# Performance work log

Measured on AMD Instinct MI355X. Metric: run time of the kernel, lower is better.

## Reference

```python
import jax, jax.numpy as jnp
import numpy as np

N_NODES = 40000
N_EDGES = 640000
D = 128


def setup_inputs() -> dict:
    key = jax.random.key(0)
    k1, k2, k3, k4, k5 = jax.random.split(key, 5)
    x = jax.random.normal(k1, (N_NODES, D), dtype=jnp.float32)
    edge_index = jax.random.randint(k2, (2, N_EDGES), 0, N_NODES, dtype=jnp.int64)
    # torch Linear stores weight as [out, in]; xavier ~ scaled normal
    scale = (2.0 / (D + D)) ** 0.5
    W_self = jax.random.normal(k3, (D, D), dtype=jnp.float32) * scale
    W_neigh = jax.random.normal(k4, (D, D), dtype=jnp.float32) * scale
    bias = jax.random.normal(k5, (D,), dtype=jnp.float32) * 0.01
    return {"x": x, "edge_index": edge_index, "W_self": W_self,
            "W_neigh": W_neigh, "bias": bias}


def reference(x, edge_index, W_self, W_neigh, bias):
    num_nodes = x.shape[0]
    row, col = edge_index[0], edge_index[1]
    # gather source features and scatter-add into destination nodes
    agg = jax.ops.segment_sum(x[row], col, num_segments=num_nodes)  # [N, D]
    deg = jax.ops.segment_sum(jnp.ones_like(col, dtype=x.dtype), col,
                              num_segments=num_nodes)
    agg = agg / jnp.clip(deg, 1.0)[:, None]
    # h_v = lin_self(x_v) + lin_neigh(mean_u x_u) + bias  (no activation in source)
    out = x @ W_self.T + agg @ W_neigh.T + bias
    return out
```

## Files before the change

kernel.cpp:

```cpp
#include <hip/hip_runtime.h>

#define N_NODES 40000
#define N_EDGES 640000
#define D 128
#define KCAT 256
#define CAP 64
#define NXCD 8
#define PART 5000
#define BUCKET_BLOCKS 1000
#define CHUNK_I4 1280

typedef __attribute__((ext_vector_type(8))) short short8v;
typedef __attribute__((ext_vector_type(4))) float f32x4;
typedef __attribute__((ext_vector_type(2))) float f32x2;


__device__ inline unsigned short f2bf(float f) {
  union { float f; unsigned int u; } v{f};
  unsigned int r = (v.u + 0x7FFFu + ((v.u >> 16) & 1u)) >> 16;
  return (unsigned short)r;
}

__global__ __launch_bounds__(256) void prep_count_kernel(
    const float* __restrict__ x, const float* __restrict__ Ws,
    const float* __restrict__ Wn, const int* __restrict__ ei, char* outb,
    unsigned short* __restrict__ Wcat, unsigned int* __restrict__ x8,
    int* __restrict__ deg, unsigned short* __restrict__ slot) {
  int b = blockIdx.x;
  int t = threadIdx.x;
  int tid = b * 256 + t;
  {
    int node = tid >> 5;
    int l = tid & 31;
    float4 v = *reinterpret_cast<const float4*>(x + (size_t)node * D + l * 4);
    ushort4 h;
    h.x = f2bf(v.x); h.y = f2bf(v.y); h.z = f2bf(v.z); h.w = f2bf(v.w);
    *reinterpret_cast<ushort4*>(outb + (size_t)node * 512 + l * 8) = h;
    unsigned int u = __builtin_amdgcn_cvt_pk_fp8_f32(v.x, v.y, 0, false);
    u = __builtin_amdgcn_cvt_pk_fp8_f32(v.z, v.w, u, true);
    x8[tid] = u;
  }
  if (tid < 8192) {
    int j = tid >> 6;
    int kq = tid & 63;
    int k0 = kq * 4;
    float4 v = (kq < 32)
        ? *reinterpret_cast<const float4*>(Ws + j * D + k0)
        : *reinterpret_cast<const float4*>(Wn + j * D + (k0 - D));
    ushort4 h;
    h.x = f2bf(v.x); h.y = f2bf(v.y); h.z = f2bf(v.z); h.w = f2bf(v.w);
    *reinterpret_cast<ushort4*>(Wcat + j * KCAT + k0) = h;
  }
  if (b < BUCKET_BLOCKS) {
    int p = b & (NXCD - 1);
    int chunk = b >> 3;
    int lo = p * PART;
    const int4* rq = reinterpret_cast<const int4*>(ei) + chunk * CHUNK_I4;
    const int4* cq =
        reinterpret_cast<const int4*>(ei + N_EDGES) + chunk * CHUNK_I4;
#pragma unroll
    for (int j = 0; j < 5; ++j) {
      int q = j * 256 + t;
      int4 r = rq[q];
      int4 c = cq[q];
      if ((unsigned)(c.x - lo) < PART)
        slot[(size_t)c.x * CAP + atomicAdd(&deg[c.x], 1)] = (unsigned short)r.x;
      if ((unsigned)(c.y - lo) < PART)
        slot[(size_t)c.y * CAP + atomicAdd(&deg[c.y], 1)] = (unsigned short)r.y;
      if ((unsigned)(c.z - lo) < PART)
        slot[(size_t)c.z * CAP + atomicAdd(&deg[c.z], 1)] = (unsigned short)r.z;
      if ((unsigned)(c.w - lo) < PART)
        slot[(size_t)c.w * CAP + atomicAdd(&deg[c.w], 1)] = (unsigned short)r.w;
    }
  }
}

__global__ __launch_bounds__(256) void gather_kernel(
    const unsigned int* __restrict__ x8, char* outb,
    const int* __restrict__ deg, const unsigned short* __restrict__ slot) {
  int node = blockIdx.x * 8 + (threadIdx.x >> 5);
  int l = threadIdx.x & 31;
  int nd = deg[node];
  const unsigned short* sp = slot + (size_t)node * CAP;
  float a0 = 0.f, a1 = 0.f, a2 = 0.f, a3 = 0.f;
  int e = 0;
  for (; e + 8 <= nd; e += 8) {
    unsigned int v[8];
#pragma unroll
    for (int j = 0; j < 8; ++j) v[j] = x8[(size_t)sp[e + j] * 32 + l];
#pragma unroll
    for (int j = 0; j < 8; ++j) {
      f32x2 lo = __builtin_amdgcn_cvt_pk_f32_fp8(v[j], false);
      f32x2 hi = __builtin_amdgcn_cvt_pk_f32_fp8(v[j], true);
      a0 += lo.x; a1 += lo.y; a2 += hi.x; a3 += hi.y;
    }
  }
  for (; e + 4 <= nd; e += 4) {
    unsigned int v[4];
#pragma unroll
    for (int j = 0; j < 4; ++j) v[j] = x8[(size_t)sp[e + j] * 32 + l];
#pragma unroll
    for (int j = 0; j < 4; ++j) {
      f32x2 lo = __builtin_amdgcn_cvt_pk_f32_fp8(v[j], false);
      f32x2 hi = __builtin_amdgcn_cvt_pk_f32_fp8(v[j], true);
      a0 += lo.x; a1 += lo.y; a2 += hi.x; a3 += hi.y;
    }
  }
  for (; e < nd; ++e) {
    unsigned int v = x8[(size_t)sp[e] * 32 + l];
    f32x2 lo = __builtin_amdgcn_cvt_pk_f32_fp8(v, false);
    f32x2 hi = __builtin_amdgcn_cvt_pk_f32_fp8(v, true);
    a0 += lo.x; a1 += lo.y; a2 += hi.x; a3 += hi.y;
  }
  float inv = 1.0f / fmaxf((float)nd, 1.0f);
  ushort4 h;
  h.x = f2bf(a0 * inv); h.y = f2bf(a1 * inv);
  h.z = f2bf(a2 * inv); h.w = f2bf(a3 * inv);
  *reinterpret_cast<ushort4*>(outb + (size_t)node * 512 + 256 + l * 8) = h;
}

__global__ __launch_bounds__(256) void sage_gemm_kernel(
    const char* ab, const unsigned short* __restrict__ Wcat,
    const float* __restrict__ bias, float* out) {
  __shared__ __align__(16) char Abuf[64 * 512];
  const int t = threadIdx.x;
  const int wave = t >> 6;
  const int lane = t & 63;
  const int node0 = blockIdx.x * 64;

  short8v breg[2][8];
#pragma unroll
  for (int jg = 0; jg < 2; ++jg) {
    int col = wave * 32 + jg * 16 + (lane & 15);
#pragma unroll
    for (int ks = 0; ks < 8; ++ks) {
      int k0 = ks * 32 + (lane >> 4) * 8;
      breg[jg][ks] =
          *reinterpret_cast<const short8v*>(Wcat + (size_t)col * KCAT + k0);
    }
  }

#pragma unroll
  for (int i = 0; i < 8; ++i) {
    int sl = i * 256 + t;
    int row = sl >> 5;
    int s = sl & 31;
    int4 v = *reinterpret_cast<const int4*>(
        ab + (size_t)(node0 + row) * 512 + s * 16);
    *reinterpret_cast<int4*>(Abuf + row * 512 + ((s ^ (row & 7)) << 4)) = v;
  }
  __syncthreads();

  const int srow = lane & 15;
  const int c7 = lane & 7;
  const int sb = lane >> 4;

  f32x4 acc[4][2] = {};
#pragma unroll
  for (int ks = 0; ks < 8; ++ks) {
    short8v af[4];
#pragma unroll
    for (int mf = 0; mf < 4; ++mf) {
      int row = mf * 16 + srow;
      int sl = (ks * 4 + sb) ^ c7;
      af[mf] = *reinterpret_cast<const short8v*>(Abuf + row * 512 + (sl << 4));
    }
#pragma unroll
    for (int mf = 0; mf < 4; ++mf)
#pragma unroll
      for (int jg = 0; jg < 2; ++jg)
        acc[mf][jg] = __builtin_amdgcn_mfma_f32_16x16x32_bf16(
            af[mf], breg[jg][ks], acc[mf][jg], 0, 0, 0);
  }
  __syncthreads();

#pragma unroll
  for (int jg = 0; jg < 2; ++jg) {
    int col = wave * 32 + jg * 16 + (lane & 15);
    float bv = bias[col];
#pragma unroll
    for (int mf = 0; mf < 4; ++mf) {
      int rbase = node0 + mf * 16 + (lane >> 4) * 4;
#pragma unroll
      for (int r = 0; r < 4; ++r) {
        out[(size_t)(rbase + r) * D + col] = acc[mf][jg][r] + bv;
      }
    }
  }
}

extern "C" void kernel_launch(void* const* d_in, const int* in_sizes, int n_in,
                              void* d_out, int out_size, void* d_ws, size_t ws_size,
                              hipStream_t stream) {
  const float* x    = (const float*)d_in[0];
  const int*   ei   = (const int*)d_in[1];
  const float* Ws   = (const float*)d_in[2];
  const float* Wn   = (const float*)d_in[3];
  const float* bias = (const float*)d_in[4];
  float* out = (float*)d_out;
  char* outb = (char*)d_out;

  unsigned short* Wcat = (unsigned short*)d_ws;
  int* deg = (int*)(Wcat + 128 * KCAT);
  unsigned short* slot = (unsigned short*)(deg + N_NODES);
  unsigned int* x8 =
      (unsigned int*)(slot + (size_t)N_NODES * CAP);

  hipMemsetAsync(deg, 0, N_NODES * sizeof(int), stream);
  prep_count_kernel<<<5000, 256, 0, stream>>>(x, Ws, Wn, ei, outb, Wcat, x8,
                                              deg, slot);
  gather_kernel<<<5000, 256, 0, stream>>>(x8, outb, deg, slot);
  sage_gemm_kernel<<<625, 256, 0, stream>>>(outb, Wcat, bias, out);
}
```

Baseline: 70.24 us.

## Convert x to bf16 inside the GEMM and spread edge bucketing across all blocks

```diff
diff --git a/kernel.cpp b/kernel.cpp
--- a/kernel.cpp
+++ b/kernel.cpp
@@ -7,8 +7,6 @@
 #define CAP 64
 #define NXCD 8
 #define PART 5000
-#define BUCKET_BLOCKS 1000
-#define CHUNK_I4 1280
 
 typedef __attribute__((ext_vector_type(8))) short short8v;
 typedef __attribute__((ext_vector_type(4))) float f32x4;
@@ -23,19 +21,14 @@
 
 __global__ __launch_bounds__(256) void prep_count_kernel(
     const float* __restrict__ x, const float* __restrict__ Ws,
-    const float* __restrict__ Wn, const int* __restrict__ ei, char* outb,
+    const float* __restrict__ Wn, const int* __restrict__ ei,
     unsigned short* __restrict__ Wcat, unsigned int* __restrict__ x8,
     int* __restrict__ deg, unsigned short* __restrict__ slot) {
   int b = blockIdx.x;
   int t = threadIdx.x;
   int tid = b * 256 + t;
   {
-    int node = tid >> 5;
-    int l = tid & 31;
-    float4 v = *reinterpret_cast<const float4*>(x + (size_t)node * D + l * 4);
-    ushort4 h;
-    h.x = f2bf(v.x); h.y = f2bf(v.y); h.z = f2bf(v.z); h.w = f2bf(v.w);
-    *reinterpret_cast<ushort4*>(outb + (size_t)node * 512 + l * 8) = h;
+    float4 v = *reinterpret_cast<const float4*>(x + (size_t)tid * 4);
     unsigned int u = __builtin_amdgcn_cvt_pk_fp8_f32(v.x, v.y, 0, false);
     u = __builtin_amdgcn_cvt_pk_fp8_f32(v.z, v.w, u, true);
     x8[tid] = u;
@@ -51,32 +44,26 @@
     h.x = f2bf(v.x); h.y = f2bf(v.y); h.z = f2bf(v.z); h.w = f2bf(v.w);
     *reinterpret_cast<ushort4*>(Wcat + j * KCAT + k0) = h;
   }
-  if (b < BUCKET_BLOCKS) {
+  {
     int p = b & (NXCD - 1);
     int chunk = b >> 3;
     int lo = p * PART;
-    const int4* rq = reinterpret_cast<const int4*>(ei) + chunk * CHUNK_I4;
-    const int4* cq =
-        reinterpret_cast<const int4*>(ei + N_EDGES) + chunk * CHUNK_I4;
-#pragma unroll
-    for (int j = 0; j < 5; ++j) {
-      int q = j * 256 + t;
-      int4 r = rq[q];
-      int4 c = cq[q];
-      if ((unsigned)(c.x - lo) < PART)
-        slot[(size_t)c.x * CAP + atomicAdd(&deg[c.x], 1)] = (unsigned short)r.x;
-      if ((unsigned)(c.y - lo) < PART)
-        slot[(size_t)c.y * CAP + atomicAdd(&deg[c.y], 1)] = (unsigned short)r.y;
-      if ((unsigned)(c.z - lo) < PART)
-        slot[(size_t)c.z * CAP + atomicAdd(&deg[c.z], 1)] = (unsigned short)r.z;
-      if ((unsigned)(c.w - lo) < PART)
-        slot[(size_t)c.w * CAP + atomicAdd(&deg[c.w], 1)] = (unsigned short)r.w;
-    }
+    int q = chunk * 256 + t;
+    int4 r = reinterpret_cast<const int4*>(ei)[q];
+    int4 c = reinterpret_cast<const int4*>(ei + N_EDGES)[q];
+    if ((unsigned)(c.x - lo) < PART)
+      slot[(size_t)c.x * CAP + atomicAdd(&deg[c.x], 1)] = (unsigned short)r.x;
+    if ((unsigned)(c.y - lo) < PART)
+      slot[(size_t)c.y * CAP + atomicAdd(&deg[c.y], 1)] = (unsigned short)r.y;
+    if ((unsigned)(c.z - lo) < PART)
+      slot[(size_t)c.z * CAP + atomicAdd(&deg[c.z], 1)] = (unsigned short)r.z;
+    if ((unsigned)(c.w - lo) < PART)
+      slot[(size_t)c.w * CAP + atomicAdd(&deg[c.w], 1)] = (unsigned short)r.w;
   }
 }
 
 __global__ __launch_bounds__(256) void gather_kernel(
-    const unsigned int* __restrict__ x8, char* outb,
+    const unsigned int* __restrict__ x8, unsigned short* __restrict__ aggb,
     const int* __restrict__ deg, const unsigned short* __restrict__ slot) {
   int node = blockIdx.x * 8 + (threadIdx.x >> 5);
   int l = threadIdx.x & 31;
@@ -116,12 +103,13 @@
   ushort4 h;
   h.x = f2bf(a0 * inv); h.y = f2bf(a1 * inv);
   h.z = f2bf(a2 * inv); h.w = f2bf(a3 * inv);
-  *reinterpret_cast<ushort4*>(outb + (size_t)node * 512 + 256 + l * 8) = h;
+  *reinterpret_cast<ushort4*>(aggb + (size_t)node * D + l * 4) = h;
 }
 
 __global__ __launch_bounds__(256) void sage_gemm_kernel(
-    const char* ab, const unsigned short* __restrict__ Wcat,
-    const float* __restrict__ bias, float* out) {
+    const float* __restrict__ x, const unsigned short* __restrict__ aggb,
+    const unsigned short* __restrict__ Wcat, const float* __restrict__ bias,
+    float* __restrict__ out) {
   __shared__ __align__(16) char Abuf[64 * 512];
   const int t = threadIdx.x;
   const int wave = t >> 6;
@@ -141,12 +129,27 @@
   }
 
 #pragma unroll
-  for (int i = 0; i < 8; ++i) {
-    int sl = i * 256 + t;
-    int row = sl >> 5;
-    int s = sl & 31;
-    int4 v = *reinterpret_cast<const int4*>(
-        ab + (size_t)(node0 + row) * 512 + s * 16);
+  for (int i = 0; i < 4; ++i) {
+    int q = i * 256 + t;
+    int row = q >> 4;
+    int s = q & 15;
+    const float* xp = x + (size_t)(node0 + row) * D + s * 8;
+    float4 v0 = *reinterpret_cast<const float4*>(xp);
+    float4 v1 = *reinterpret_cast<const float4*>(xp + 4);
+    ushort4 h0, h1;
+    h0.x = f2bf(v0.x); h0.y = f2bf(v0.y); h0.z = f2bf(v0.z); h0.w = f2bf(v0.w);
+    h1.x = f2bf(v1.x); h1.y = f2bf(v1.y); h1.z = f2bf(v1.z); h1.w = f2bf(v1.w);
+    char* dst = Abuf + row * 512 + ((s ^ (row & 7)) << 4);
+    *reinterpret_cast<ushort4*>(dst) = h0;
+    *reinterpret_cast<ushort4*>(dst + 8) = h1;
+  }
+#pragma unroll
+  for (int i = 0; i < 4; ++i) {
+    int q = i * 256 + t;
+    int row = q >> 4;
+    int s = 16 + (q & 15);
+    int4 v = *reinterpret_cast<const int4*>(aggb + (size_t)(node0 + row) * D +
+                                            (q & 15) * 8);
     *reinterpret_cast<int4*>(Abuf + row * 512 + ((s ^ (row & 7)) << 4)) = v;
   }
   __syncthreads();
@@ -172,7 +175,6 @@
         acc[mf][jg] = __builtin_amdgcn_mfma_f32_16x16x32_bf16(
             af[mf], breg[jg][ks], acc[mf][jg], 0, 0, 0);
   }
-  __syncthreads();
 
 #pragma unroll
   for (int jg = 0; jg < 2; ++jg) {
@@ -198,17 +200,18 @@
   const float* Wn   = (const float*)d_in[3];
   const float* bias = (const float*)d_in[4];
   float* out = (float*)d_out;
-  char* outb = (char*)d_out;
 
   unsigned short* Wcat = (unsigned short*)d_ws;
   int* deg = (int*)(Wcat + 128 * KCAT);
   unsigned short* slot = (unsigned short*)(deg + N_NODES);
   unsigned int* x8 =
       (unsigned int*)(slot + (size_t)N_NODES * CAP);
+  unsigned short* aggb =
+      (unsigned short*)(x8 + (size_t)N_NODES * 32);
 
   hipMemsetAsync(deg, 0, N_NODES * sizeof(int), stream);
-  prep_count_kernel<<<5000, 256, 0, stream>>>(x, Ws, Wn, ei, outb, Wcat, x8,
-                                              deg, slot);
-  gather_kernel<<<5000, 256, 0, stream>>>(x8, outb, deg, slot);
-  sage_gemm_kernel<<<625, 256, 0, stream>>>(outb, Wcat, bias, out);
-}
+  prep_count_kernel<<<5000, 256, 0, stream>>>(x, Ws, Wn, ei, Wcat, x8, deg,
+                                              slot);
+  gather_kernel<<<5000, 256, 0, stream>>>(x8, aggb, deg, slot);
+  sage_gemm_kernel<<<625, 256, 0, stream>>>(x, aggb, Wcat, bias, out);
+}
```

After: 70.68 us. Within noise of the previous version (+0.6%).
